# Performance work log

Hardware: AMD Instinct MI355X
Metric: run time of the kernel (lower is better)

The kernel has to match this reference:

```python
import jax, jax.numpy as jnp
import numpy as np

G = 8          # attention groups (n_heads)
LN_EPS = 1e-5  # torch nn.LayerNorm default eps


def setup_inputs() -> dict:
    key = jax.random.key(0)
    ks = jax.random.split(key, 9)
    B, T, Fin, D, O, K = 4, 4096, 229, 256, 88, 31
    return {
        "spec": jax.random.normal(ks[0], (B, T, Fin), dtype=jnp.float32),
        "W_q": jax.random.normal(ks[1], (D, Fin), dtype=jnp.float32) * 0.05,
        "W_k": jax.random.normal(ks[2], (D, Fin), dtype=jnp.float32) * 0.05,
        "W_v": jax.random.normal(ks[3], (D, Fin), dtype=jnp.float32) * 0.05,
        "rel": jax.random.normal(ks[4], (1, D, K), dtype=jnp.float32),
        "ln_gamma": jnp.ones((D,), dtype=jnp.float32),
        "ln_beta": jnp.zeros((D,), dtype=jnp.float32),
        "lin_w": jax.random.normal(ks[5], (O, D), dtype=jnp.float32) * 0.05,
        "lin_b": jnp.zeros((O,), dtype=jnp.float32),
    }


def reference(spec, W_q, W_k, W_v, rel, ln_gamma, ln_beta, lin_w, lin_b):
    B, T, Fin = spec.shape
    D = W_q.shape[0]
    K = rel.shape[-1]
    pad = (K - 1) // 2
    Dg = D // G

    # projections (padding time dim for k/v as in F.pad(x, [0,0,pad,pad]))
    q = spec @ W_q.T                                   # [B,T,D]
    padded = jnp.pad(spec, ((0, 0), (pad, pad), (0, 0)))
    k = padded @ W_k.T                                 # [B,T+K-1,D]
    v = padded @ W_v.T

    # sliding windows (torch unfold, stride 1): window t covers frames t..t+K-1
    idx = jnp.arange(T)[:, None] + jnp.arange(K)[None, :]   # [T,K]
    k_w = k[:, idx] + rel[0].T                         # [B,T,K,D] (+rel bias [K,D])
    v_w = v[:, idx]                                    # [B,T,K,D]

    # split channels into groups: [B,T,K,G,Dg]
    kg = k_w.reshape(B, T, K, G, Dg)
    vg = v_w.reshape(B, T, K, G, Dg)
    qg = q.reshape(B, T, G, Dg)

    energy = jnp.einsum('btgd,btkgd->btgk', qg, kg)    # [B,T,G,K]
    attn = jax.nn.softmax(energy, axis=-1)
    out = jnp.einsum('btgk,btkgd->btgd', attn, vg).reshape(B, T, D)

    # LayerNorm (biased variance, as torch)
    mu = out.mean(-1, keepdims=True)
    var = ((out - mu) ** 2).mean(-1, keepdims=True)
    h = (out - mu) / jnp.sqrt(var + LN_EPS) * ln_gamma + ln_beta

    frame_pred = jax.nn.sigmoid(h @ lin_w.T + lin_b)   # [B,T,O]
    return frame_pred, attn
```

## Files before the change

kernel.cpp:

```cpp
#include <hip/hip_runtime.h>
#include <hip/hip_bf16.h>

typedef unsigned int uint;
typedef unsigned short ushort;

#define B_ 4
#define T_ 4096
#define FIN 229
#define D_ 256
#define O_ 88
#define KW 31
#define G_ 8
#define LN_EPS 1e-5f
#define SBW 464
#define W2W 512

typedef __attribute__((ext_vector_type(8))) short short8;
typedef __attribute__((ext_vector_type(4))) float f32x4;

__device__ __forceinline__ ushort f2bf(float x) {
  uint u = __float_as_uint(x);
  uint r = (u + 0x7fffu + ((u >> 16) & 1u)) >> 16;
  return (ushort)r;
}
__device__ __forceinline__ float bflo(uint u) { return __uint_as_float(u << 16); }
__device__ __forceinline__ float bfhi(uint u) { return __uint_as_float(u & 0xffff0000u); }

__global__ __launch_bounds__(256) void conv_spec(const float* __restrict__ spec,
                                                 ushort* __restrict__ specB) {
  int row = blockIdx.x;
  int f = threadIdx.x;
  if (f >= 232) return;
  float x = (f < FIN) ? spec[(long)row * FIN + f] : 0.f;
  ushort hi = f2bf(x);
  ushort lo = f2bf(x - bflo((uint)hi));
  specB[(long)row * SBW + f] = hi;
  specB[(long)row * SBW + 232 + f] = lo;
}

__global__ __launch_bounds__(256) void conv_w2(const float* __restrict__ Wq,
                                               const float* __restrict__ Wk,
                                               const float* __restrict__ Wv,
                                               ushort* __restrict__ W2) {
  int d3 = blockIdx.x;
  int f = threadIdx.x;
  const float* src = (d3 < 256) ? Wq : (d3 < 512 ? Wk : Wv);
  int dr = d3 & 255;
  float x = (f < FIN) ? src[dr * FIN + f] : 0.f;
  ushort hi = f2bf(x);
  ushort lo = f2bf(x - bflo((uint)hi));
  W2[(long)d3 * W2W + f] = hi;
  W2[(long)d3 * W2W + 256 + f] = lo;
}

__global__ __launch_bounds__(256) void conv_lw(const float* __restrict__ lw,
                                               ushort* __restrict__ lwB) {
  int o = blockIdx.x;
  int d = threadIdx.x;
  lwB[o * 256 + d] = (o < O_) ? f2bf(lw[o * 256 + d]) : (ushort)0;
}

#define KSTEPS 24
__global__ __launch_bounds__(256) void proj_mfma(const ushort* __restrict__ specB,
                                                 const ushort* __restrict__ W2,
                                                 float* __restrict__ qb,
                                                 float* __restrict__ kb,
                                                 ushort* __restrict__ vb) {
  __shared__ ushort As[128 * 32];
  __shared__ ushort Bs[128 * 32];
  int tid = threadIdx.x;
  int lane = tid & 63, w = tid >> 6;
  int bm = blockIdx.x, bn = blockIdx.y;
  int l15 = lane & 15, kg = lane >> 4;
  int rS = tid >> 1, cS = (tid & 1) * 16;

  const ushort* arow = specB + (long)(bm * 128 + rS) * SBW;
  const ushort* brow = W2 + (long)(bn * 128 + rS) * W2W;

  f32x4 acc[2][8];
  #pragma unroll
  for (int mi = 0; mi < 2; ++mi)
    #pragma unroll
    for (int nf = 0; nf < 8; ++nf)
      acc[mi][nf] = (f32x4){0.f, 0.f, 0.f, 0.f};

  for (int s = 0; s < KSTEPS; ++s) {
    int seg = s >> 3;
    int f0 = (s & 7) * 32;
    int acol = (seg == 1 ? 232 : 0) + f0;
    int bcol = (seg == 2 ? 256 : 0) + f0;

    uint4 a0 = *(const uint4*)(arow + acol + cS);
    uint4 a1 = *(const uint4*)(arow + acol + cS + 8);
    uint4 b0 = *(const uint4*)(brow + bcol + cS);
    uint4 b1 = *(const uint4*)(brow + bcol + cS + 8);
    __syncthreads();
    *(uint4*)(&As[rS * 32 + cS]) = a0;
    *(uint4*)(&As[rS * 32 + cS + 8]) = a1;
    *(uint4*)(&Bs[rS * 32 + cS]) = b0;
    *(uint4*)(&Bs[rS * 32 + cS + 8]) = b1;
    __syncthreads();

    short8 af[2];
    af[0] = *(const short8*)(&As[(w * 32 + l15) * 32 + kg * 8]);
    af[1] = *(const short8*)(&As[(w * 32 + 16 + l15) * 32 + kg * 8]);
    short8 bfr[8];
    #pragma unroll
    for (int nf = 0; nf < 8; ++nf)
      bfr[nf] = *(const short8*)(&Bs[(nf * 16 + l15) * 32 + kg * 8]);
    #pragma unroll
    for (int mi = 0; mi < 2; ++mi)
      #pragma unroll
      for (int nf = 0; nf < 8; ++nf)
        acc[mi][nf] = __builtin_amdgcn_mfma_f32_16x16x32_bf16(af[mi], bfr[nf], acc[mi][nf], 0, 0, 0);
  }

  #pragma unroll
  for (int mi = 0; mi < 2; ++mi)
    #pragma unroll
    for (int nf = 0; nf < 8; ++nf)
      #pragma unroll
      for (int ic = 0; ic < 4; ++ic) {
        int row = bm * 128 + w * 32 + mi * 16 + kg * 4 + ic;
        int col = bn * 128 + nf * 16 + l15;
        float val = acc[mi][nf][ic];
        if (bn < 2) {
          qb[(long)row * 256 + col] = val;
        } else if (bn < 4) {
          kb[(long)row * 256 + (col - 256)] = val;
        } else {
          vb[(long)row * 256 + (col - 512)] = f2bf(val);
        }
      }
}

#define TROWS 8
#define KROWS 39
#define KS_OFF 0
#define VS_OFF 40576
#define QS_OFF 60544
#define AS_OFF 68864
#define HS_OFF 0
#define SM_BYTES 72960

__global__ __launch_bounds__(256) void attn4(
    const float* __restrict__ qb, const float* __restrict__ kb,
    const ushort* __restrict__ vb, const float* __restrict__ rel,
    const float* __restrict__ lng, const float* __restrict__ lnb,
    ushort* __restrict__ hB, float* __restrict__ attn) {
  __shared__ alignas(16) char sm[SM_BYTES];

  int tid = threadIdx.x;
  int b = blockIdx.y;
  int t0 = blockIdx.x * TROWS;
  long bT = (long)b * T_;
  int g = tid >> 5;
  int j = tid & 31;

  for (int idx = tid; idx < KROWS * 64; idx += 256) {
    int r = idx >> 6, c4 = idx & 63;
    int grow = t0 + r - 15;
    float4 kv = make_float4(0.f, 0.f, 0.f, 0.f);
    if ((unsigned)grow < (unsigned)T_)
      kv = *(const float4*)(kb + (bT + grow) * 256 + c4 * 4);
    *(float4*)(sm + KS_OFF + r * 1040 + c4 * 16) = kv;
  }
  for (int idx = tid; idx < KROWS * 32; idx += 256) {
    int r = idx >> 5, c16 = idx & 31;
    int grow = t0 + r - 15;
    uint4 vv = {0u, 0u, 0u, 0u};
    if ((unsigned)grow < (unsigned)T_)
      vv = *(const uint4*)(vb + (bT + grow) * 256 + c16 * 8);
    *(uint4*)(sm + VS_OFF + ((r * 512 + c16 * 16) ^ ((r & 7) << 4))) = vv;
  }
  for (int idx = tid; idx < TROWS * 64; idx += 256) {
    int r = idx >> 6, c4 = idx & 63;
    float4 qv = *(const float4*)(qb + (bT + t0 + r) * 256 + c4 * 4);
    *(float4*)(sm + QS_OFF + r * 1040 + c4 * 16) = qv;
  }
  float relf[32];
  #pragma unroll
  for (int c = 0; c < 32; ++c)
    relf[c] = (j < KW) ? rel[(g * 32 + c) * 31 + j] : 0.f;
  __syncthreads();

  ushort* aS = (ushort*)(sm + AS_OFF);
  #pragma unroll 1
  for (int i = 0; i < TROWS; ++i) {
    int row = i + j;
    float ek0 = 0.f, ek1 = 0.f, ek2 = 0.f, ek3 = 0.f;
    float er0 = 0.f, er1 = 0.f, er2 = 0.f, er3 = 0.f;
    #pragma unroll
    for (int c = 0; c < 4; ++c) {
      float4 ka = *(const float4*)(sm + KS_OFF + row * 1040 + g * 128 + c * 32);
      float4 kc = *(const float4*)(sm + KS_OFF + row * 1040 + g * 128 + c * 32 + 16);
      float4 qa = *(const float4*)(sm + QS_OFF + i * 1040 + g * 128 + c * 32);
      float4 qc = *(const float4*)(sm + QS_OFF + i * 1040 + g * 128 + c * 32 + 16);
      ek0 += qa.x * ka.x + qa.y * ka.y;
      ek1 += qa.z * ka.z + qa.w * ka.w;
      ek2 += qc.x * kc.x + qc.y * kc.y;
      ek3 += qc.z * kc.z + qc.w * kc.w;
      er0 += qa.x * relf[c * 8 + 0] + qa.y * relf[c * 8 + 1];
      er1 += qa.z * relf[c * 8 + 2] + qa.w * relf[c * 8 + 3];
      er2 += qc.x * relf[c * 8 + 4] + qc.y * relf[c * 8 + 5];
      er3 += qc.z * relf[c * 8 + 6] + qc.w * relf[c * 8 + 7];
    }
    float e = ((ek0 + ek1) + (ek2 + ek3)) + ((er0 + er1) + (er2 + er3));
    float ev = (j < KW) ? e : -3.4e38f;
    float m = ev;
    m = fmaxf(m, __shfl_xor(m, 16)); m = fmaxf(m, __shfl_xor(m, 8));
    m = fmaxf(m, __shfl_xor(m, 4));  m = fmaxf(m, __shfl_xor(m, 2));
    m = fmaxf(m, __shfl_xor(m, 1));
    float ex = (j < KW) ? __expf(ev - m) : 0.f;
    float ssum = ex;
    ssum += __shfl_xor(ssum, 16); ssum += __shfl_xor(ssum, 8);
    ssum += __shfl_xor(ssum, 4);  ssum += __shfl_xor(ssum, 2);
    ssum += __shfl_xor(ssum, 1);
    float a = ex / ssum;
    aS[(i * 8 + g) * 32 + j] = f2bf(a);
    if (j < KW) attn[((bT + t0 + i) * 8 + g) * 31 + j] = a;
  }
  __syncthreads();

  {
    int tsub = j >> 3;
    int d8 = (j & 7) * 8;
    #pragma unroll
    for (int ii = 0; ii < 2; ++ii) {
      int tq = ii * 4 + tsub;
      float o0 = 0.f, o1 = 0.f, o2 = 0.f, o3 = 0.f;
      #pragma unroll
      for (int kp4 = 0; kp4 < 8; ++kp4) {
        uint2 a4 = *(const uint2*)(sm + AS_OFF + (tq * 8 + g) * 64 + kp4 * 8);
        float a0 = bflo(a4.x), a1 = bfhi(a4.x), a2 = bflo(a4.y), a3 = bfhi(a4.y);
        #pragma unroll
        for (int c = 0; c < 4; ++c) {
          float ac = (c == 0) ? a0 : (c == 1) ? a1 : (c == 2) ? a2 : a3;
          int row = tq + kp4 * 4 + c;
          uint2 v4 = *(const uint2*)(sm + VS_OFF + ((row * 512 + g * 64 + d8) ^ ((row & 7) << 4)));
          o0 += ac * bflo(v4.x);
          o1 += ac * bfhi(v4.x);
          o2 += ac * bflo(v4.y);
          o3 += ac * bfhi(v4.y);
        }
      }
      *(float4*)(sm + HS_OFF + tq * 1040 + g * 128 + (j & 7) * 16) = make_float4(o0, o1, o2, o3);
    }
  }
  __syncthreads();

  float4 x0 = *(const float4*)(sm + HS_OFF + g * 1040 + j * 32);
  float4 x1 = *(const float4*)(sm + HS_OFF + g * 1040 + j * 32 + 16);
  float s1 = x0.x + x0.y + x0.z + x0.w + x1.x + x1.y + x1.z + x1.w;
  float s2 = x0.x * x0.x + x0.y * x0.y + x0.z * x0.z + x0.w * x0.w +
             x1.x * x1.x + x1.y * x1.y + x1.z * x1.z + x1.w * x1.w;
  s1 += __shfl_xor(s1, 16); s2 += __shfl_xor(s2, 16);
  s1 += __shfl_xor(s1, 8);  s2 += __shfl_xor(s2, 8);
  s1 += __shfl_xor(s1, 4);  s2 += __shfl_xor(s2, 4);
  s1 += __shfl_xor(s1, 2);  s2 += __shfl_xor(s2, 2);
  s1 += __shfl_xor(s1, 1);  s2 += __shfl_xor(s2, 1);
  float mu = s1 * (1.f / 256.f);
  float var = s2 * (1.f / 256.f) - mu * mu;
  float inv = rsqrtf(var + LN_EPS);
  float4 ga = *(const float4*)(lng + j * 8);
  float4 gb = *(const float4*)(lng + j * 8 + 4);
  float4 ba = *(const float4*)(lnb + j * 8);
  float4 bb = *(const float4*)(lnb + j * 8 + 4);
  uint4 hp;
  hp.x = (uint)f2bf((x0.x - mu) * inv * ga.x + ba.x) |
         ((uint)f2bf((x0.y - mu) * inv * ga.y + ba.y) << 16);
  hp.y = (uint)f2bf((x0.z - mu) * inv * ga.z + ba.z) |
         ((uint)f2bf((x0.w - mu) * inv * ga.w + ba.w) << 16);
  hp.z = (uint)f2bf((x1.x - mu) * inv * gb.x + bb.x) |
         ((uint)f2bf((x1.y - mu) * inv * gb.y + bb.y) << 16);
  hp.w = (uint)f2bf((x1.z - mu) * inv * gb.z + bb.z) |
         ((uint)f2bf((x1.w - mu) * inv * gb.w + bb.w) << 16);
  *(uint4*)(hB + (bT + t0 + g) * 256 + j * 8) = hp;
}

__global__ __launch_bounds__(256) void lin_mfma(const ushort* __restrict__ hB,
                                                const ushort* __restrict__ lwB,
                                                const float* __restrict__ lb,
                                                float* __restrict__ frame) {
  __shared__ ushort As[64 * 32];
  __shared__ ushort Bs[96 * 264];
  int tid = threadIdx.x;
  int lane = tid & 63, w = tid >> 6;
  int blk = blockIdx.x;
  int l15 = lane & 15, kg = lane >> 4;

  for (int idx = tid; idx < 96 * 32; idx += 256) {
    int o = idx >> 5, c8 = idx & 31;
    uint4 bv = *(const uint4*)(lwB + o * 256 + c8 * 8);
    *(uint4*)(&Bs[o * 264 + c8 * 8]) = bv;
  }

  f32x4 acc[6];
  #pragma unroll
  for (int nf = 0; nf < 6; ++nf) acc[nf] = (f32x4){0.f, 0.f, 0.f, 0.f};

  for (int s = 0; s < 8; ++s) {
    uint4 a0 = {0u, 0u, 0u, 0u}, a1 = {0u, 0u, 0u, 0u};
    if (tid < 128) {
      const ushort* hp = hB + (long)(blk * 64 + (tid >> 1)) * 256 + s * 32 + (tid & 1) * 16;
      a0 = *(const uint4*)(hp);
      a1 = *(const uint4*)(hp + 8);
    }
    __syncthreads();
    if (tid < 128) {
      *(uint4*)(&As[(tid >> 1) * 32 + (tid & 1) * 16]) = a0;
      *(uint4*)(&As[(tid >> 1) * 32 + (tid & 1) * 16 + 8]) = a1;
    }
    __syncthreads();

    short8 af = *(const short8*)(&As[(w * 16 + l15) * 32 + kg * 8]);
    #pragma unroll
    for (int nf = 0; nf < 6; ++nf) {
      short8 bf = *(const short8*)(&Bs[(nf * 16 + l15) * 264 + s * 32 + kg * 8]);
      acc[nf] = __builtin_amdgcn_mfma_f32_16x16x32_bf16(af, bf, acc[nf], 0, 0, 0);
    }
  }

  #pragma unroll
  for (int nf = 0; nf < 6; ++nf) {
    int col = nf * 16 + l15;
    if (col < O_) {
      float bo = lb[col];
      #pragma unroll
      for (int ic = 0; ic < 4; ++ic) {
        int row = blk * 64 + w * 16 + kg * 4 + ic;
        float z = acc[nf][ic] + bo;
        frame[(long)row * O_ + col] = 1.f / (1.f + __expf(-z));
      }
    }
  }
}

extern "C" void kernel_launch(void* const* d_in, const int* in_sizes, int n_in,
                              void* d_out, int out_size, void* d_ws, size_t ws_size,
                              hipStream_t stream) {
  const float* spec = (const float*)d_in[0];
  const float* Wq   = (const float*)d_in[1];
  const float* Wk   = (const float*)d_in[2];
  const float* Wv   = (const float*)d_in[3];
  const float* rel  = (const float*)d_in[4];
  const float* lng  = (const float*)d_in[5];
  const float* lnb  = (const float*)d_in[6];
  const float* lw   = (const float*)d_in[7];
  const float* lb   = (const float*)d_in[8];

  float* out   = (float*)d_out;
  float* frame = out;
  float* attn  = out + (long)B_ * T_ * O_;

  char* ws = (char*)d_ws;
  float*  qb    = (float*)ws;
  float*  kb    = (float*)(ws + (16u << 20));
  ushort* vb    = (ushort*)(ws + (32u << 20));
  ushort* specB = (ushort*)(ws + (40u << 20));
  ushort* W2    = (ushort*)(ws + (40u << 20) + 15204352u);
  ushort* lwB   = (ushort*)(ws + (40u << 20) + 15204352u + 786432u);
  ushort* hB    = specB;

  conv_spec<<<16384, 256, 0, stream>>>(spec, specB);
  conv_w2<<<768, 256, 0, stream>>>(Wq, Wk, Wv, W2);
  conv_lw<<<96, 256, 0, stream>>>(lw, lwB);
  proj_mfma<<<dim3(128, 6), 256, 0, stream>>>(specB, W2, qb, kb, vb);
  attn4<<<dim3(512, 4), 256, 0, stream>>>(qb, kb, vb, rel, lng, lnb, hB, attn);
  lin_mfma<<<256, 256, 0, stream>>>(hB, lwB, lb, frame);
}
```

Baseline: 214.2 us.

## Vectorize spec conversion, prefetch and pad GEMM tiles, enlarge attention tile

```diff
diff --git a/kernel.cpp b/kernel.cpp
--- a/kernel.cpp
+++ b/kernel.cpp
@@ -28,14 +28,34 @@
 
 __global__ __launch_bounds__(256) void conv_spec(const float* __restrict__ spec,
                                                  ushort* __restrict__ specB) {
-  int row = blockIdx.x;
-  int f = threadIdx.x;
-  if (f >= 232) return;
-  float x = (f < FIN) ? spec[(long)row * FIN + f] : 0.f;
-  ushort hi = f2bf(x);
-  ushort lo = f2bf(x - bflo((uint)hi));
-  specB[(long)row * SBW + f] = hi;
-  specB[(long)row * SBW + 232 + f] = lo;
+  int tid = threadIdx.x;
+  int r = tid >> 5, c = tid & 31;
+  if (c >= 29) return;
+  long row = (long)blockIdx.x * 8 + r;
+  const float* sp = spec + row * FIN + c * 8;
+  float x[8];
+  #pragma unroll
+  for (int u = 0; u < 8; ++u) {
+    int f = c * 8 + u;
+    x[u] = (f < FIN) ? sp[u] : 0.f;
+  }
+  ushort hi[8], lo[8];
+  #pragma unroll
+  for (int u = 0; u < 8; ++u) {
+    hi[u] = f2bf(x[u]);
+    lo[u] = f2bf(x[u] - bflo((uint)hi[u]));
+  }
+  uint4 hp, lp;
+  hp.x = (uint)hi[0] | ((uint)hi[1] << 16);
+  hp.y = (uint)hi[2] | ((uint)hi[3] << 16);
+  hp.z = (uint)hi[4] | ((uint)hi[5] << 16);
+  hp.w = (uint)hi[6] | ((uint)hi[7] << 16);
+  lp.x = (uint)lo[0] | ((uint)lo[1] << 16);
+  lp.y = (uint)lo[2] | ((uint)lo[3] << 16);
+  lp.z = (uint)lo[4] | ((uint)lo[5] << 16);
+  lp.w = (uint)lo[6] | ((uint)lo[7] << 16);
+  *(uint4*)(specB + row * SBW + c * 8) = hp;
+  *(uint4*)(specB + row * SBW + 232 + c * 8) = lp;
 }
 
 __global__ __launch_bounds__(256) void conv_w2(const float* __restrict__ Wq,
@@ -66,8 +86,8 @@
                                                  float* __restrict__ qb,
                                                  float* __restrict__ kb,
                                                  ushort* __restrict__ vb) {
-  __shared__ ushort As[128 * 32];
-  __shared__ ushort Bs[128 * 32];
+  __shared__ ushort As[128 * 40];
+  __shared__ ushort Bs[128 * 40];
   int tid = threadIdx.x;
   int lane = tid & 63, w = tid >> 6;
   int bm = blockIdx.x, bn = blockIdx.y;
@@ -84,30 +104,41 @@
     for (int nf = 0; nf < 8; ++nf)
       acc[mi][nf] = (f32x4){0.f, 0.f, 0.f, 0.f};
 
+  uint4 a0, a1, b0, b1;
+  {
+    a0 = *(const uint4*)(arow + cS);
+    a1 = *(const uint4*)(arow + cS + 8);
+    b0 = *(const uint4*)(brow + cS);
+    b1 = *(const uint4*)(brow + cS + 8);
+  }
+
   for (int s = 0; s < KSTEPS; ++s) {
-    int seg = s >> 3;
-    int f0 = (s & 7) * 32;
-    int acol = (seg == 1 ? 232 : 0) + f0;
-    int bcol = (seg == 2 ? 256 : 0) + f0;
-
-    uint4 a0 = *(const uint4*)(arow + acol + cS);
-    uint4 a1 = *(const uint4*)(arow + acol + cS + 8);
-    uint4 b0 = *(const uint4*)(brow + bcol + cS);
-    uint4 b1 = *(const uint4*)(brow + bcol + cS + 8);
     __syncthreads();
-    *(uint4*)(&As[rS * 32 + cS]) = a0;
-    *(uint4*)(&As[rS * 32 + cS + 8]) = a1;
-    *(uint4*)(&Bs[rS * 32 + cS]) = b0;
-    *(uint4*)(&Bs[rS * 32 + cS + 8]) = b1;
+    *(uint4*)(&As[rS * 40 + cS]) = a0;
+    *(uint4*)(&As[rS * 40 + cS + 8]) = a1;
+    *(uint4*)(&Bs[rS * 40 + cS]) = b0;
+    *(uint4*)(&Bs[rS * 40 + cS + 8]) = b1;
     __syncthreads();
 
+    if (s + 1 < KSTEPS) {
+      int sn = s + 1;
+      int seg = sn >> 3;
+      int f0 = (sn & 7) * 32;
+      int acol = (seg == 1 ? 232 : 0) + f0;
+      int bcol = (seg == 2 ? 256 : 0) + f0;
+      a0 = *(const uint4*)(arow + acol + cS);
+      a1 = *(const uint4*)(arow + acol + cS + 8);
+      b0 = *(const uint4*)(brow + bcol + cS);
+      b1 = *(const uint4*)(brow + bcol + cS + 8);
+    }
+
     short8 af[2];
-    af[0] = *(const short8*)(&As[(w * 32 + l15) * 32 + kg * 8]);
-    af[1] = *(const short8*)(&As[(w * 32 + 16 + l15) * 32 + kg * 8]);
+    af[0] = *(const short8*)(&As[(w * 32 + l15) * 40 + kg * 8]);
+    af[1] = *(const short8*)(&As[(w * 32 + 16 + l15) * 40 + kg * 8]);
     short8 bfr[8];
     #pragma unroll
     for (int nf = 0; nf < 8; ++nf)
-      bfr[nf] = *(const short8*)(&Bs[(nf * 16 + l15) * 32 + kg * 8]);
+      bfr[nf] = *(const short8*)(&Bs[(nf * 16 + l15) * 40 + kg * 8]);
     #pragma unroll
     for (int mi = 0; mi < 2; ++mi)
       #pragma unroll
@@ -134,16 +165,16 @@
       }
 }
 
-#define TROWS 8
-#define KROWS 39
+#define TROWS 16
+#define KROWS 47
 #define KS_OFF 0
-#define VS_OFF 40576
-#define QS_OFF 60544
-#define AS_OFF 68864
+#define VS_OFF 48896
+#define QS_OFF 72960
+#define AS_OFF 89600
 #define HS_OFF 0
-#define SM_BYTES 72960
-
-__global__ __launch_bounds__(256) void attn4(
+#define SM_BYTES 97792
+
+__global__ __launch_bounds__(512) void attn4(
     const float* __restrict__ qb, const float* __restrict__ kb,
     const ushort* __restrict__ vb, const float* __restrict__ rel,
     const float* __restrict__ lng, const float* __restrict__ lnb,
@@ -154,10 +185,12 @@
   int b = blockIdx.y;
   int t0 = blockIdx.x * TROWS;
   long bT = (long)b * T_;
-  int g = tid >> 5;
+  int h = tid >> 5;
   int j = tid & 31;
-
-  for (int idx = tid; idx < KROWS * 64; idx += 256) {
+  int g = h & 7;
+  int ibase = (h >> 3) * 8;
+
+  for (int idx = tid; idx < KROWS * 64; idx += 512) {
     int r = idx >> 6, c4 = idx & 63;
     int grow = t0 + r - 15;
     float4 kv = make_float4(0.f, 0.f, 0.f, 0.f);
@@ -165,7 +198,7 @@
       kv = *(const float4*)(kb + (bT + grow) * 256 + c4 * 4);
     *(float4*)(sm + KS_OFF + r * 1040 + c4 * 16) = kv;
   }
-  for (int idx = tid; idx < KROWS * 32; idx += 256) {
+  for (int idx = tid; idx < KROWS * 32; idx += 512) {
     int r = idx >> 5, c16 = idx & 31;
     int grow = t0 + r - 15;
     uint4 vv = {0u, 0u, 0u, 0u};
@@ -173,7 +206,7 @@
       vv = *(const uint4*)(vb + (bT + grow) * 256 + c16 * 8);
     *(uint4*)(sm + VS_OFF + ((r * 512 + c16 * 16) ^ ((r & 7) << 4))) = vv;
   }
-  for (int idx = tid; idx < TROWS * 64; idx += 256) {
+  for (int idx = tid; idx < TROWS * 64; idx += 512) {
     int r = idx >> 6, c4 = idx & 63;
     float4 qv = *(const float4*)(qb + (bT + t0 + r) * 256 + c4 * 4);
     *(float4*)(sm + QS_OFF + r * 1040 + c4 * 16) = qv;
@@ -186,7 +219,8 @@
 
   ushort* aS = (ushort*)(sm + AS_OFF);
   #pragma unroll 1
-  for (int i = 0; i < TROWS; ++i) {
+  for (int ii = 0; ii < 8; ++ii) {
+    int i = ibase + ii;
     int row = i + j;
     float ek0 = 0.f, ek1 = 0.f, ek2 = 0.f, ek3 = 0.f;
     float er0 = 0.f, er1 = 0.f, er2 = 0.f, er3 = 0.f;
@@ -227,7 +261,7 @@
     int d8 = (j & 7) * 8;
     #pragma unroll
     for (int ii = 0; ii < 2; ++ii) {
-      int tq = ii * 4 + tsub;
+      int tq = (h >> 3) * 8 + ii * 4 + tsub;
       float o0 = 0.f, o1 = 0.f, o2 = 0.f, o3 = 0.f;
       #pragma unroll
       for (int kp4 = 0; kp4 < 8; ++kp4) {
@@ -249,8 +283,8 @@
   }
   __syncthreads();
 
-  float4 x0 = *(const float4*)(sm + HS_OFF + g * 1040 + j * 32);
-  float4 x1 = *(const float4*)(sm + HS_OFF + g * 1040 + j * 32 + 16);
+  float4 x0 = *(const float4*)(sm + HS_OFF + h * 1040 + j * 32);
+  float4 x1 = *(const float4*)(sm + HS_OFF + h * 1040 + j * 32 + 16);
   float s1 = x0.x + x0.y + x0.z + x0.w + x1.x + x1.y + x1.z + x1.w;
   float s2 = x0.x * x0.x + x0.y * x0.y + x0.z * x0.z + x0.w * x0.w +
              x1.x * x1.x + x1.y * x1.y + x1.z * x1.z + x1.w * x1.w;
@@ -275,14 +309,14 @@
          ((uint)f2bf((x1.y - mu) * inv * gb.y + bb.y) << 16);
   hp.w = (uint)f2bf((x1.z - mu) * inv * gb.z + bb.z) |
          ((uint)f2bf((x1.w - mu) * inv * gb.w + bb.w) << 16);
-  *(uint4*)(hB + (bT + t0 + g) * 256 + j * 8) = hp;
+  *(uint4*)(hB + (bT + t0 + h) * 256 + j * 8) = hp;
 }
 
 __global__ __launch_bounds__(256) void lin_mfma(const ushort* __restrict__ hB,
                                                 const ushort* __restrict__ lwB,
                                                 const float* __restrict__ lb,
                                                 float* __restrict__ frame) {
-  __shared__ ushort As[64 * 32];
+  __shared__ ushort As[64 * 40];
   __shared__ ushort Bs[96 * 264];
   int tid = threadIdx.x;
   int lane = tid & 63, w = tid >> 6;
@@ -308,12 +342,12 @@
     }
     __syncthreads();
     if (tid < 128) {
-      *(uint4*)(&As[(tid >> 1) * 32 + (tid & 1) * 16]) = a0;
-      *(uint4*)(&As[(tid >> 1) * 32 + (tid & 1) * 16 + 8]) = a1;
+      *(uint4*)(&As[(tid >> 1) * 40 + (tid & 1) * 16]) = a0;
+      *(uint4*)(&As[(tid >> 1) * 40 + (tid & 1) * 16 + 8]) = a1;
     }
     __syncthreads();
 
-    short8 af = *(const short8*)(&As[(w * 16 + l15) * 32 + kg * 8]);
+    short8 af = *(const short8*)(&As[(w * 16 + l15) * 40 + kg * 8]);
     #pragma unroll
     for (int nf = 0; nf < 6; ++nf) {
       short8 bf = *(const short8*)(&Bs[(nf * 16 + l15) * 264 + s * 32 + kg * 8]);
@@ -362,10 +396,10 @@
   ushort* lwB   = (ushort*)(ws + (40u << 20) + 15204352u + 786432u);
   ushort* hB    = specB;
 
-  conv_spec<<<16384, 256, 0, stream>>>(spec, specB);
+  conv_spec<<<2048, 256, 0, stream>>>(spec, specB);
   conv_w2<<<768, 256, 0, stream>>>(Wq, Wk, Wv, W2);
   conv_lw<<<96, 256, 0, stream>>>(lw, lwB);
   proj_mfma<<<dim3(128, 6), 256, 0, stream>>>(specB, W2, qb, kb, vb);
-  attn4<<<dim3(512, 4), 256, 0, stream>>>(qb, kb, vb, rel, lng, lnb, hB, attn);
+  attn4<<<dim3(256, 4), 512, 0, stream>>>(qb, kb, vb, rel, lng, lnb, hB, attn);
   lin_mfma<<<256, 256, 0, stream>>>(hB, lwB, lb, frame);
 }
```

Result: faster. 193.4 us (-9.7%).
